# Kernel tuning notes

Hardware: AMD Instinct MI355X
Metric: run time of the kernel (lower is better)

The kernel has to match this reference:

```python
import jax, jax.numpy as jnp
import numpy as np

B, SQ, SK, H, HEADS, E, DFF = 4, 512, 1024, 1024, 16, 8, 4096
DH = H // HEADS
EPS = 1e-6


def _ln(x, g, b):
    m = jnp.mean(x, -1, keepdims=True)
    v = jnp.mean((x - m) ** 2, -1, keepdims=True)
    return (x - m) * jax.lax.rsqrt(v + EPS) * g + b


def setup_inputs() -> dict:
    key = jax.random.key(0)
    ks = jax.random.split(key, 16)
    s = 0.02
    return {
        "concated_input": jax.random.normal(ks[0], (B, SK, H), jnp.float32),
        "gen_emb": jax.random.normal(ks[1], (B, SQ, H), jnp.float32),
        "mask": jnp.zeros((B, 1, SQ, SK), jnp.float32),
        "ln_g": jnp.ones((H,), jnp.float32),
        "ln_b": jnp.zeros((H,), jnp.float32),
        "wq": jax.random.normal(ks[2], (H, H), jnp.float32) * s,
        "bq": jnp.zeros((H,), jnp.float32),
        "wk": jax.random.normal(ks[3], (H, H), jnp.float32) * s,
        "bk": jnp.zeros((H,), jnp.float32),
        "wv": jax.random.normal(ks[4], (H, H), jnp.float32) * s,
        "bv": jnp.zeros((H,), jnp.float32),
        "wo": jax.random.normal(ks[5], (H, H), jnp.float32) * s,
        "bo": jnp.zeros((H,), jnp.float32),
        "gw": jax.random.normal(ks[6], (H, E), jnp.float32) * s,
        "gb": jnp.zeros((E,), jnp.float32),
        "w1": jax.random.normal(ks[7], (E, H, DFF), jnp.float32) * s,
        "b1": jnp.zeros((E, DFF), jnp.float32),
        "w2": jax.random.normal(ks[8], (E, DFF, H), jnp.float32) * s,
        "b2": jnp.zeros((E, H), jnp.float32),
    }


def reference(concated_input, gen_emb, mask, ln_g, ln_b, wq, bq, wk, bk, wv, bv,
              wo, bo, gw, gb, w1, b1, w2, b2):
    residual_gen = gen_emb
    ctx_ln = _ln(concated_input, ln_g, ln_b)
    gen_ln = _ln(gen_emb, ln_g, ln_b)

    # multi-head cross attention: gen queries, concated keys/values
    q = (gen_ln @ wq + bq).reshape(B, SQ, HEADS, DH).transpose(0, 2, 1, 3)
    k = (ctx_ln @ wk + bk).reshape(B, SK, HEADS, DH).transpose(0, 2, 1, 3)
    v = (ctx_ln @ wv + bv).reshape(B, SK, HEADS, DH).transpose(0, 2, 1, 3)
    scores = jnp.einsum("bhqd,bhkd->bhqk", q, k) / np.sqrt(DH).astype(np.float32)
    attn = jax.nn.softmax(scores + mask, axis=-1)
    ctx_v = jnp.einsum("bhqk,bhkd->bhqd", attn, v)
    ctx_v = ctx_v.transpose(0, 2, 1, 3).reshape(B, SQ, H)
    ca_out = ctx_v @ wo + bo + residual_gen

    ln_ca = _ln(ca_out, ln_g, ln_b)

    # top-1 router on ca_out (pre-LN, as in original)
    gate = jax.nn.softmax(ca_out @ gw + gb, axis=-1)
    top_idx = jnp.argmax(gate, axis=-1)  # [B,SQ]

    # dense all-expert FFN, then gather selected expert (faithful to original)
    h1 = jax.nn.gelu(jnp.einsum("bsh,ehf->bsef", ln_ca, w1) + b1, approximate=False)
    expert_out = jnp.einsum("bsef,efh->bseh", h1, w2) + b2  # [B,SQ,E,H]
    sel = jnp.take_along_axis(expert_out, top_idx[:, :, None, None], axis=2)
    moe_out = sel[:, :, 0, :] + ln_ca
    return moe_out
```

## Files before the change

kernel.cpp:

```cpp
#include <hip/hip_runtime.h>
#include <stdint.h>
#include <stddef.h>

typedef _Float16 f16;
typedef _Float16 half8 __attribute__((ext_vector_type(8)));
typedef float f32x4 __attribute__((ext_vector_type(4)));

constexpr int kB = 4, kSQ = 512, kSK = 1024, kH = 1024, kHeads = 16, kE = 8, kDFF = 4096;
constexpr int kTok = kB * kSQ;

__device__ __forceinline__ void g2l16(const f16* g, f16* l) {
  __builtin_amdgcn_global_load_lds((const __attribute__((address_space(1))) uint32_t*)g,
                                   (__attribute__((address_space(3))) uint32_t*)l, 16, 0, 0);
}

__global__ __launch_bounds__(256) void tr_f2h(const float* __restrict__ src,
                                              f16* __restrict__ dst, int R, int C) {
  __shared__ float t[32][33];
  long zo = (long)blockIdx.z * R * C;
  int r0 = blockIdx.y * 32, c0 = blockIdx.x * 32;
  int tr = threadIdx.x >> 3, tc = (threadIdx.x & 7) << 2;
  float4 v = *(const float4*)(src + zo + (long)(r0 + tr) * C + c0 + tc);
  t[tr][tc] = v.x; t[tr][tc + 1] = v.y; t[tr][tc + 2] = v.z; t[tr][tc + 3] = v.w;
  __syncthreads();
  union { f16 h[4]; uint2 u; } o;
  o.h[0] = (f16)t[tc + 0][tr]; o.h[1] = (f16)t[tc + 1][tr];
  o.h[2] = (f16)t[tc + 2][tr]; o.h[3] = (f16)t[tc + 3][tr];
  *(uint2*)(dst + zo + (long)(c0 + tr) * R + r0 + tc) = o.u;
}

__global__ __launch_bounds__(256) void ln_kernel(const float* __restrict__ x,
                                                 const float* __restrict__ g,
                                                 const float* __restrict__ b,
                                                 f16* __restrict__ oh, float* __restrict__ of,
                                                 int rows) {
  int row = blockIdx.x;
  if (row >= rows) return;
  int tid = threadIdx.x;
  const float* xr = x + (long)row * kH;
  float4 v = *(const float4*)(xr + tid * 4);
  float s = v.x + v.y + v.z + v.w;
  float s2 = v.x * v.x + v.y * v.y + v.z * v.z + v.w * v.w;
  __shared__ float red[8];
  for (int o = 32; o; o >>= 1) { s += __shfl_down(s, o); s2 += __shfl_down(s2, o); }
  int wv = tid >> 6, lane = tid & 63;
  if (lane == 0) { red[wv] = s; red[4 + wv] = s2; }
  __syncthreads();
  if (tid == 0) {
    red[0] = red[0] + red[1] + red[2] + red[3];
    red[4] = red[4] + red[5] + red[6] + red[7];
  }
  __syncthreads();
  float mean = red[0] * (1.0f / kH);
  float var = red[4] * (1.0f / kH) - mean * mean;
  float rs = rsqrtf(var + 1e-6f);
  float4 gv = *(const float4*)(g + tid * 4);
  float4 bv = *(const float4*)(b + tid * 4);
  float y0 = (v.x - mean) * rs * gv.x + bv.x;
  float y1 = (v.y - mean) * rs * gv.y + bv.y;
  float y2 = (v.z - mean) * rs * gv.z + bv.z;
  float y3 = (v.w - mean) * rs * gv.w + bv.w;
  long base = (long)row * kH + tid * 4;
  if (oh) {
    union { f16 h[4]; uint2 u; } o;
    o.h[0] = (f16)y0; o.h[1] = (f16)y1; o.h[2] = (f16)y2; o.h[3] = (f16)y3;
    *(uint2*)(oh + base) = o.u;
  }
  if (of) { float4 o4 = {y0, y1, y2, y3}; *(float4*)(of + base) = o4; }
}

__global__ void zero_kernel(int* __restrict__ p, int n) {
  int i = blockIdx.x * blockDim.x + threadIdx.x;
  if (i < n) p[i] = 0;
}

__global__ __launch_bounds__(64) void router_kernel(const float* __restrict__ ca,
                                                    const float* __restrict__ gw,
                                                    const float* __restrict__ gb,
                                                    int* __restrict__ cursors,
                                                    int* __restrict__ list,
                                                    int* __restrict__ eid) {
  int t = blockIdx.x;
  int lane = threadIdx.x;
  const float* x = ca + (long)t * kH;
  float acc[kE];
#pragma unroll
  for (int e = 0; e < kE; e++) acc[e] = 0.0f;
  for (int h = lane; h < kH; h += 64) {
    float xv = x[h];
    const float* gr = gw + (long)h * kE;
#pragma unroll
    for (int e = 0; e < kE; e++) acc[e] += xv * gr[e];
  }
#pragma unroll
  for (int e = 0; e < kE; e++)
    for (int o = 32; o; o >>= 1) acc[e] += __shfl_down(acc[e], o);
  if (lane == 0) {
    int best = 0;
    float bv = acc[0] + gb[0];
    for (int e = 1; e < kE; e++) {
      float v = acc[e] + gb[e];
      if (v > bv) { bv = v; best = e; }
    }
    int slot = atomicAdd(&cursors[best], 1);
    list[best * kTok + slot] = t;
    eid[t] = best;
  }
}

__global__ __launch_bounds__(256) void ffn2_reduce(const float* __restrict__ part,
                                                   const float* __restrict__ lnca,
                                                   const float* __restrict__ b2,
                                                   const int* __restrict__ eid,
                                                   float* __restrict__ out) {
  int t = blockIdx.x;
  int i = threadIdx.x * 4;
  int e = eid[t];
  long idx = (long)t * kH + i;
  float4 p0 = *(const float4*)(part + idx);
  float4 p1 = *(const float4*)(part + (long)kTok * kH + idx);
  float4 p2 = *(const float4*)(part + 2L * kTok * kH + idx);
  float4 p3 = *(const float4*)(part + 3L * kTok * kH + idx);
  float4 r  = *(const float4*)(lnca + idx);
  float4 bb = *(const float4*)(b2 + (long)e * kH + i);
  float4 o = {p0.x + p1.x + p2.x + p3.x + r.x + bb.x,
              p0.y + p1.y + p2.y + p3.y + r.y + bb.y,
              p0.z + p1.z + p2.z + p3.z + r.z + bb.z,
              p0.w + p1.w + p2.w + p3.w + r.w + bb.w};
  *(float4*)(out + idx) = o;
}

__global__ __launch_bounds__(256) void flash_kernel(const f16* __restrict__ q,
                                                    const f16* __restrict__ k,
                                                    const f16* __restrict__ v_t,
                                                    const float* __restrict__ mask,
                                                    f16* __restrict__ ctx) {
  __shared__ f16 Ks[64 * 64];
  __shared__ f16 Vs[64 * 64];
  __shared__ f16 Ps[4][16][72];
  int qt = blockIdx.x;
  int bh = blockIdx.y;
  int b = bh >> 4;
  int ho = (bh & 15) * 64;
  int tid = threadIdx.x, lane = tid & 63, wave = tid >> 6;
  int quad = lane >> 4, lo = lane & 15;

  long qg = ((long)b * kSQ + qt * 64 + wave * 16 + lo) * kH + ho;
  half8 aq0 = *(const half8*)(q + qg + quad * 8);
  half8 aq1 = *(const half8*)(q + qg + 32 + quad * 8);

  int srow = tid >> 3;
  int soct = (tid & 7) ^ (srow & 7);
  const f16* ksrc[2];
  const f16* vsrc[2];
#pragma unroll
  for (int s = 0; s < 2; s++) {
    int r = s * 32 + srow;
    ksrc[s] = k + ((long)b * kSK + r) * kH + ho + soct * 8;
    vsrc[s] = v_t + ((long)bh * 64 + r) * kSK + soct * 8;
  }
  const float* maskp = mask + ((long)b * kSQ + qt * 64 + wave * 16 + quad * 4) * kSK;

  float m_s[4] = {-1e30f, -1e30f, -1e30f, -1e30f};
  float l_s[4] = {0.f, 0.f, 0.f, 0.f};
  f32x4 O[4] = {};

  for (int kt = 0; kt < kSK / 64; kt++) {
    int sk0 = kt * 64;
#pragma unroll
    for (int s = 0; s < 2; s++) g2l16(ksrc[s] + (long)sk0 * kH, &Ks[(s * 256 + tid) * 8]);
#pragma unroll
    for (int s = 0; s < 2; s++) g2l16(vsrc[s] + sk0, &Vs[(s * 256 + tid) * 8]);
    __syncthreads();
    f32x4 sf[4] = {};
#pragma unroll
    for (int nt = 0; nt < 4; nt++) {
      int key = nt * 16 + lo;
      half8 bk0 = *(const half8*)&Ks[key * 64 + (((0 * 4 + quad)) ^ (key & 7)) * 8];
      half8 bk1 = *(const half8*)&Ks[key * 64 + (((1 * 4 + quad)) ^ (key & 7)) * 8];
      sf[nt] = __builtin_amdgcn_mfma_f32_16x16x32_f16(aq0, bk0, sf[nt], 0, 0, 0);
      sf[nt] = __builtin_amdgcn_mfma_f32_16x16x32_f16(aq1, bk1, sf[nt], 0, 0, 0);
    }
#pragma unroll
    for (int r = 0; r < 4; r++)
#pragma unroll
      for (int nt = 0; nt < 4; nt++)
        sf[nt][r] += maskp[(long)r * kSK + sk0 + nt * 16 + lo];
#pragma unroll
    for (int r = 0; r < 4; r++) {
      float mx = fmaxf(fmaxf(sf[0][r], sf[1][r]), fmaxf(sf[2][r], sf[3][r]));
      mx = fmaxf(mx, __shfl_xor(mx, 1));
      mx = fmaxf(mx, __shfl_xor(mx, 2));
      mx = fmaxf(mx, __shfl_xor(mx, 4));
      mx = fmaxf(mx, __shfl_xor(mx, 8));
      float m_new = fmaxf(m_s[r], mx);
      float alpha = __expf(m_s[r] - m_new);
      m_s[r] = m_new;
      float p0 = __expf(sf[0][r] - m_new), p1 = __expf(sf[1][r] - m_new);
      float p2 = __expf(sf[2][r] - m_new), p3 = __expf(sf[3][r] - m_new);
      float rs = p0 + p1 + p2 + p3;
      rs += __shfl_xor(rs, 1);
      rs += __shfl_xor(rs, 2);
      rs += __shfl_xor(rs, 4);
      rs += __shfl_xor(rs, 8);
      l_s[r] = l_s[r] * alpha + rs;
#pragma unroll
      for (int nt = 0; nt < 4; nt++) O[nt][r] *= alpha;
      Ps[wave][quad * 4 + r][0 * 16 + lo] = (f16)p0;
      Ps[wave][quad * 4 + r][1 * 16 + lo] = (f16)p1;
      Ps[wave][quad * 4 + r][2 * 16 + lo] = (f16)p2;
      Ps[wave][quad * 4 + r][3 * 16 + lo] = (f16)p3;
    }
    half8 ap0 = *(const half8*)&Ps[wave][lo][quad * 8];
    half8 ap1 = *(const half8*)&Ps[wave][lo][32 + quad * 8];
#pragma unroll
    for (int nt = 0; nt < 4; nt++) {
      int d = nt * 16 + lo;
      half8 bv0 = *(const half8*)&Vs[d * 64 + (((0 * 4 + quad)) ^ (d & 7)) * 8];
      half8 bv1 = *(const half8*)&Vs[d * 64 + (((1 * 4 + quad)) ^ (d & 7)) * 8];
      O[nt] = __builtin_amdgcn_mfma_f32_16x16x32_f16(ap0, bv0, O[nt], 0, 0, 0);
      O[nt] = __builtin_amdgcn_mfma_f32_16x16x32_f16(ap1, bv1, O[nt], 0, 0, 0);
    }
    __syncthreads();
  }
#pragma unroll
  for (int r = 0; r < 4; r++) {
    float inv = 1.0f / l_s[r];
    long row = (long)b * kSQ + qt * 64 + wave * 16 + quad * 4 + r;
#pragma unroll
    for (int nt = 0; nt < 4; nt++)
      ctx[row * kH + ho + nt * 16 + lo] = (f16)(O[nt][r] * inv);
  }
}

struct GemmP {
  const f16* A; long a_row, a_z1, a_z2;
  const f16* Bm; long b_nstr, b_z1, b_z2;
  float* Cf; f16* Ch; long c_row, c_z1, c_z2, c_split; int c_tr;
  const float* bias; long bias_z;
  const float* res; long res_row, res_z1, res_z2;
  float alpha; int gelu; int ksplit;
  int M, N, K, zdiv;
  const int* glist; const int* cnt;
};

template <int BM, int BN>
__device__ __forceinline__ void gemm_body(const GemmP& p, int bx, int by, int bz,
                                          f16* A0, f16* A1, f16* B0, f16* B1) {
  constexpr int FM = BM / 32, FN = BN / 32;
  int z = bz;
  int kb = 0, kEnd = p.K, ks = 0;
  if (p.ksplit > 1) {
    int kc = p.K / p.ksplit;
    ks = z % p.ksplit;
    kb = ks * kc;
    kEnd = kb + kc;
    z /= p.ksplit;
  }
  long aoff = 0, boff = 0, coff = 0, roff = 0, biasoff = 0;
  const int* gl = nullptr;
  int Meff = p.M;
  if (p.glist) {
    Meff = p.cnt[z];
    gl = p.glist + (long)z * kTok;
    boff = (long)z * p.b_z2;
    biasoff = (long)z * p.bias_z;
  } else {
    int z1 = z / p.zdiv, z2 = z % p.zdiv;
    aoff = (long)z1 * p.a_z1 + (long)z2 * p.a_z2;
    boff = (long)z1 * p.b_z1 + (long)z2 * p.b_z2;
    coff = (long)z1 * p.c_z1 + (long)z2 * p.c_z2;
    roff = (long)z1 * p.res_z1 + (long)z2 * p.res_z2;
  }
  coff += (long)ks * p.c_split;
  int m0 = by * BM;
  if (m0 >= Meff) return;
  int n0 = bx * BN;
  int tid = threadIdx.x, lane = tid & 63, wave = tid >> 6;
  int wm = (wave & 1) * (BM / 2), wn = (wave >> 1) * (BN / 2);
  int q = lane >> 4, lo = lane & 15;

  int srow = tid >> 3;
  int soct = (tid & 7) ^ (srow & 7);
  const f16* asrc[BM / 32];
  const f16* bsrc[BN / 32];
#pragma unroll
  for (int s = 0; s < BM / 32; s++) {
    int row = m0 + s * 32 + srow;
    if (gl) row = gl[row < Meff ? row : Meff - 1];
    asrc[s] = p.A + aoff + (long)row * p.a_row + soct * 8;
  }
#pragma unroll
  for (int s = 0; s < BN / 32; s++)
    bsrc[s] = p.Bm + boff + (long)(n0 + s * 32 + srow) * p.b_nstr + soct * 8;

  f32x4 acc[FM][FN] = {};

  auto stage = [&](f16* Ad, f16* Bd, int k0) {
#pragma unroll
    for (int s = 0; s < BM / 32; s++) g2l16(asrc[s] + k0, &Ad[(s * 256 + tid) * 8]);
#pragma unroll
    for (int s = 0; s < BN / 32; s++) g2l16(bsrc[s] + k0, &Bd[(s * 256 + tid) * 8]);
  };
  auto compute = [&](const f16* As, const f16* Bs) {
    half8 af[2][FM], bf[2][FN];
#pragma unroll
    for (int kk = 0; kk < 2; kk++) {
#pragma unroll
      for (int i = 0; i < FM; i++) {
        int r = wm + i * 16 + lo;
        af[kk][i] = *(const half8*)&As[r * 64 + ((kk * 4 + q) ^ (r & 7)) * 8];
      }
#pragma unroll
      for (int j = 0; j < FN; j++) {
        int n = wn + j * 16 + lo;
        bf[kk][j] = *(const half8*)&Bs[n * 64 + ((kk * 4 + q) ^ (n & 7)) * 8];
      }
    }
#pragma unroll
    for (int kk = 0; kk < 2; kk++)
#pragma unroll
      for (int i = 0; i < FM; i++)
#pragma unroll
        for (int j = 0; j < FN; j++)
          acc[i][j] = __builtin_amdgcn_mfma_f32_16x16x32_f16(af[kk][i], bf[kk][j], acc[i][j], 0, 0, 0);
  };

  stage(A0, B0, kb);
  __syncthreads();
  for (int k0 = kb; k0 < kEnd; k0 += 128) {
    if (k0 + 64 < kEnd) stage(A1, B1, k0 + 64);
    compute(A0, B0);
    __syncthreads();
    if (k0 + 64 < kEnd) {
      if (k0 + 128 < kEnd) stage(A0, B0, k0 + 128);
      compute(A1, B1);
      __syncthreads();
    }
  }

#pragma unroll
  for (int i = 0; i < FM; i++) {
#pragma unroll
    for (int j = 0; j < FN; j++) {
      int col = n0 + wn + j * 16 + lo;
      if (p.c_tr) {
        int row0 = m0 + wm + i * 16 + q * 4;
        union { f16 h[4]; uint2 u; } o;
#pragma unroll
        for (int r = 0; r < 4; r++) {
          float v = acc[i][j][r];
          if (p.bias) v += p.bias[biasoff + col];
          v *= p.alpha;
          o.h[r] = (f16)v;
        }
        *(uint2*)&p.Ch[coff + (long)col * p.c_row + row0] = o.u;
      } else {
#pragma unroll
        for (int r = 0; r < 4; r++) {
          int row = m0 + wm + i * 16 + q * 4 + r;
          if (row < Meff) {
            long rr = gl ? (long)gl[row] : (long)row;
            float v = acc[i][j][r];
            if (p.bias) v += p.bias[biasoff + col];
            v *= p.alpha;
            if (p.res) v += p.res[roff + rr * p.res_row + col];
            if (p.gelu) v = 0.5f * v * (1.0f + erff(v * 0.70710678118654752f));
            long ci = coff + rr * p.c_row + col;
            if (p.Cf) p.Cf[ci] = v;
            else p.Ch[ci] = (f16)v;
          }
        }
      }
    }
  }
}

template <int BM, int BN>
__global__ __launch_bounds__(256) void gemm_t(GemmP p) {
  __shared__ f16 A0[BM * 64], A1[BM * 64], B0[BN * 64], B1[BN * 64];
  gemm_body<BM, BN>(p, blockIdx.x, blockIdx.y, blockIdx.z, A0, A1, B0, B1);
}

struct Multi3P {
  GemmP g0, g1, g2;
  int n0, n1;
  int gx0, gy0, gx1, gy1, gx2, gy2;
};

__global__ __launch_bounds__(256) void gemm_qkv(Multi3P mp) {
  __shared__ f16 A0[128 * 64], A1[128 * 64], B0[128 * 64], B1[128 * 64];
  int fb = blockIdx.x;
  if (fb < mp.n0) {
    gemm_body<128, 128>(mp.g0, fb % mp.gx0, (fb / mp.gx0) % mp.gy0, fb / (mp.gx0 * mp.gy0),
                        A0, A1, B0, B1);
    return;
  }
  fb -= mp.n0;
  if (fb < mp.n1) {
    gemm_body<128, 128>(mp.g1, fb % mp.gx1, (fb / mp.gx1) % mp.gy1, fb / (mp.gx1 * mp.gy1),
                        A0, A1, B0, B1);
    return;
  }
  fb -= mp.n1;
  gemm_body<128, 128>(mp.g2, fb % mp.gx2, (fb / mp.gx2) % mp.gy2, fb / (mp.gx2 * mp.gy2),
                      A0, A1, B0, B1);
}

extern "C" void kernel_launch(void* const* d_in, const int* in_sizes, int n_in,
                              void* d_out, int out_size, void* d_ws, size_t ws_size,
                              hipStream_t stream) {
  const float* concated = (const float*)d_in[0];
  const float* gen      = (const float*)d_in[1];
  const float* mask     = (const float*)d_in[2];
  const float* ln_g     = (const float*)d_in[3];
  const float* ln_b     = (const float*)d_in[4];
  const float* wq = (const float*)d_in[5];  const float* bq = (const float*)d_in[6];
  const float* wk = (const float*)d_in[7];  const float* bk = (const float*)d_in[8];
  const float* wv = (const float*)d_in[9];  const float* bv = (const float*)d_in[10];
  const float* wo = (const float*)d_in[11]; const float* bo = (const float*)d_in[12];
  const float* gw = (const float*)d_in[13]; const float* gb = (const float*)d_in[14];
  const float* w1 = (const float*)d_in[15]; const float* b1 = (const float*)d_in[16];
  const float* w2 = (const float*)d_in[17]; const float* b2 = (const float*)d_in[18];
  float* out = (float*)d_out;

  size_t off = 0;
  auto alloc = [&](size_t bytes) -> void* {
    void* p = (char*)d_ws + off;
    off += (bytes + 255) & ~(size_t)255;
    return p;
  };
  f16* wq_t  = (f16*)alloc((size_t)kH * kH * 2);
  f16* wk_t  = (f16*)alloc((size_t)kH * kH * 2);
  f16* wv_t  = (f16*)alloc((size_t)kH * kH * 2);
  f16* wo_t  = (f16*)alloc((size_t)kH * kH * 2);
  f16* w1_t  = (f16*)alloc((size_t)kE * kH * kDFF * 2);
  f16* w2_t  = (f16*)alloc((size_t)kE * kDFF * kH * 2);
  f16* lnc_h = (f16*)alloc((size_t)kB * kSK * kH * 2);
  f16* lng_h = (f16*)alloc((size_t)kTok * kH * 2);
  f16* q_h   = (f16*)alloc((size_t)kTok * kH * 2);
  f16* k_h   = (f16*)alloc((size_t)kB * kSK * kH * 2);
  f16* v_t   = (f16*)alloc((size_t)kB * kSK * kH * 2);
  f16* ctx_h = (f16*)alloc((size_t)kTok * kH * 2);
  float* ca_f   = (float*)alloc((size_t)kTok * kH * 4);
  float* lnca_f = (float*)alloc((size_t)kTok * kH * 4);
  f16* lnca_h   = (f16*)alloc((size_t)kTok * kH * 2);
  f16* h1_h     = (f16*)alloc((size_t)kTok * kDFF * 2);
  float* part_f = (float*)alloc((size_t)4 * kTok * kH * 4);
  int* cnt_d    = (int*)alloc(kE * 4);
  int* list_d   = (int*)alloc((size_t)kE * kTok * 4);
  int* eid_d    = (int*)alloc((size_t)kTok * 4);

  tr_f2h<<<dim3(32, 32, 1), 256, 0, stream>>>(wq, wq_t, kH, kH);
  tr_f2h<<<dim3(32, 32, 1), 256, 0, stream>>>(wk, wk_t, kH, kH);
  tr_f2h<<<dim3(32, 32, 1), 256, 0, stream>>>(wv, wv_t, kH, kH);
  tr_f2h<<<dim3(32, 32, 1), 256, 0, stream>>>(wo, wo_t, kH, kH);
  tr_f2h<<<dim3(kDFF / 32, kH / 32, kE), 256, 0, stream>>>(w1, w1_t, kH, kDFF);
  tr_f2h<<<dim3(kH / 32, kDFF / 32, kE), 256, 0, stream>>>(w2, w2_t, kDFF, kH);

  ln_kernel<<<kB * kSK, 256, 0, stream>>>(concated, ln_g, ln_b, lnc_h, nullptr, kB * kSK);
  ln_kernel<<<kTok, 256, 0, stream>>>(gen, ln_g, ln_b, lng_h, nullptr, kTok);

  {
    Multi3P mp{};
    GemmP& pq = mp.g0;
    pq.A = lng_h; pq.a_row = kH; pq.Bm = wq_t; pq.b_nstr = kH;
    pq.Ch = q_h; pq.c_row = kH; pq.bias = bq; pq.alpha = 0.125f;
    pq.M = kTok; pq.N = kH; pq.K = kH; pq.zdiv = 1;
    GemmP& pk = mp.g1;
    pk.A = lnc_h; pk.a_row = kH; pk.Bm = wk_t; pk.b_nstr = kH;
    pk.Ch = k_h; pk.c_row = kH; pk.bias = bk; pk.alpha = 1.0f;
    pk.M = kB * kSK; pk.N = kH; pk.K = kH; pk.zdiv = 1;
    GemmP& pv = mp.g2;
    pv.A = lnc_h; pv.a_row = kH; pv.a_z1 = (long)kSK * kH;
    pv.Bm = wv_t; pv.b_nstr = kH;
    pv.Ch = v_t; pv.c_row = kSK; pv.c_z1 = (long)kH * kSK; pv.c_tr = 1;
    pv.bias = bv; pv.alpha = 1.0f;
    pv.M = kSK; pv.N = kH; pv.K = kH; pv.zdiv = 1;
    mp.gx0 = kH / 128; mp.gy0 = kTok / 128;        mp.n0 = mp.gx0 * mp.gy0;
    mp.gx1 = kH / 128; mp.gy1 = (kB * kSK) / 128;  mp.n1 = mp.gx1 * mp.gy1;
    mp.gx2 = kH / 128; mp.gy2 = kSK / 128;
    int ntot = mp.n0 + mp.n1 + mp.gx2 * mp.gy2 * kB;
    gemm_qkv<<<dim3(ntot), 256, 0, stream>>>(mp);
  }
  flash_kernel<<<dim3(kSQ / 64, kB * kHeads), 256, 0, stream>>>(q_h, k_h, v_t, mask, ctx_h);
  {
    GemmP p{}; p.A = ctx_h; p.a_row = kH;
    p.Bm = wo_t; p.b_nstr = kH;
    p.Cf = ca_f; p.c_row = kH; p.bias = bo;
    p.res = gen; p.res_row = kH;
    p.alpha = 1.0f; p.M = kTok; p.N = kH; p.K = kH; p.zdiv = 1;
    gemm_t<64, 64><<<dim3(kH / 64, kTok / 64, 1), 256, 0, stream>>>(p);
  }
  ln_kernel<<<kTok, 256, 0, stream>>>(ca_f, ln_g, ln_b, lnca_h, lnca_f, kTok);
  zero_kernel<<<1, 64, 0, stream>>>(cnt_d, kE);
  router_kernel<<<kTok, 64, 0, stream>>>(ca_f, gw, gb, cnt_d, list_d, eid_d);
  {
    GemmP p{}; p.A = lnca_h; p.a_row = kH;
    p.Bm = w1_t; p.b_nstr = kH; p.b_z2 = (long)kH * kDFF;
    p.Ch = h1_h; p.c_row = kDFF; p.bias = b1; p.bias_z = kDFF;
    p.alpha = 1.0f; p.gelu = 1; p.M = kTok; p.N = kDFF; p.K = kH; p.zdiv = 1;
    p.glist = list_d; p.cnt = cnt_d;
    gemm_t<128, 128><<<dim3(kDFF / 128, kTok / 128, kE), 256, 0, stream>>>(p);
  }
  {
    GemmP p{}; p.A = h1_h; p.a_row = kDFF;
    p.Bm = w2_t; p.b_nstr = kDFF; p.b_z2 = (long)kDFF * kH;
    p.Cf = part_f; p.c_row = kH; p.c_split = (long)kTok * kH;
    p.alpha = 1.0f; p.ksplit = 4;
    p.M = kTok; p.N = kH; p.K = kDFF; p.zdiv = 1;
    p.glist = list_d; p.cnt = cnt_d;
    gemm_t<128, 128><<<dim3(kH / 128, kTok / 128, kE * 4), 256, 0, stream>>>(p);
  }
  ffn2_reduce<<<kTok, 256, 0, stream>>>(part_f, lnca_f, b2, eid_d, out);
}
```

Baseline: 690.1 us.

## Triple-buffer GEMM K-loop with vmcnt waits and switch tiles to 128x64

Replaces the double-buffered K loop, which had two full barriers per pair of stages, with a three-buffer ring. Each iteration issues loads two tiles ahead, waits on the vmcnt counter only for the current tile, and uses a single barrier. All GEMM launches move to 128x64 tiles, which gives more blocks and keeps LDS use near the old 128x128 double-buffered footprint. The aim is deeper load/compute overlap and better occupancy. The cost is half the MMA work per B-tile load and a hand-counted vmcnt that must match the number of loads issued per stage.

```diff
diff --git a/kernel.cpp b/kernel.cpp
--- a/kernel.cpp
+++ b/kernel.cpp
@@ -12,6 +12,11 @@
 __device__ __forceinline__ void g2l16(const f16* g, f16* l) {
   __builtin_amdgcn_global_load_lds((const __attribute__((address_space(1))) uint32_t*)g,
                                    (__attribute__((address_space(3))) uint32_t*)l, 16, 0, 0);
+}
+
+template <int N>
+__device__ __forceinline__ void vmwait() {
+  asm volatile("s_waitcnt vmcnt(%0)" :: "i"(N) : "memory");
 }
 
 __global__ __launch_bounds__(256) void tr_f2h(const float* __restrict__ src,
@@ -246,8 +251,10 @@
 
 template <int BM, int BN>
 __device__ __forceinline__ void gemm_body(const GemmP& p, int bx, int by, int bz,
-                                          f16* A0, f16* A1, f16* B0, f16* B1) {
+                                          f16* A0, f16* A1, f16* A2,
+                                          f16* B0, f16* B1, f16* B2) {
   constexpr int FM = BM / 32, FN = BN / 32;
+  constexpr int PER = BM / 32 + BN / 32;
   int z = bz;
   int kb = 0, kEnd = p.K, ks = 0;
   if (p.ksplit > 1) {
@@ -326,17 +333,20 @@
           acc[i][j] = __builtin_amdgcn_mfma_f32_16x16x32_f16(af[kk][i], bf[kk][j], acc[i][j], 0, 0, 0);
   };
 
+  int nt = (kEnd - kb) / 64;
   stage(A0, B0, kb);
-  __syncthreads();
-  for (int k0 = kb; k0 < kEnd; k0 += 128) {
-    if (k0 + 64 < kEnd) stage(A1, B1, k0 + 64);
-    compute(A0, B0);
-    __syncthreads();
-    if (k0 + 64 < kEnd) {
-      if (k0 + 128 < kEnd) stage(A0, B0, k0 + 128);
-      compute(A1, B1);
-      __syncthreads();
-    }
+  if (nt > 1) stage(A1, B1, kb + 64);
+  f16 *Ac = A0, *An = A1, *Af = A2;
+  f16 *Bc = B0, *Bn = B1, *Bf = B2;
+  for (int i = 0; i < nt; i++) {
+    if (i + 1 < nt) vmwait<PER>(); else vmwait<0>();
+    __builtin_amdgcn_sched_barrier(0);
+    __builtin_amdgcn_s_barrier();
+    if (i + 2 < nt) stage(Af, Bf, kb + (i + 2) * 64);
+    compute(Ac, Bc);
+    f16* t;
+    t = Ac; Ac = An; An = Af; Af = t;
+    t = Bc; Bc = Bn; Bn = Bf; Bf = t;
   }
 
 #pragma unroll
@@ -378,8 +388,9 @@
 
 template <int BM, int BN>
 __global__ __launch_bounds__(256) void gemm_t(GemmP p) {
-  __shared__ f16 A0[BM * 64], A1[BM * 64], B0[BN * 64], B1[BN * 64];
-  gemm_body<BM, BN>(p, blockIdx.x, blockIdx.y, blockIdx.z, A0, A1, B0, B1);
+  __shared__ f16 A0[BM * 64], A1[BM * 64], A2[BM * 64];
+  __shared__ f16 B0[BN * 64], B1[BN * 64], B2[BN * 64];
+  gemm_body<BM, BN>(p, blockIdx.x, blockIdx.y, blockIdx.z, A0, A1, A2, B0, B1, B2);
 }
 
 struct Multi3P {
@@ -389,22 +400,23 @@
 };
 
 __global__ __launch_bounds__(256) void gemm_qkv(Multi3P mp) {
-  __shared__ f16 A0[128 * 64], A1[128 * 64], B0[128 * 64], B1[128 * 64];
+  __shared__ f16 A0[128 * 64], A1[128 * 64], A2[128 * 64];
+  __shared__ f16 B0[64 * 64], B1[64 * 64], B2[64 * 64];
   int fb = blockIdx.x;
   if (fb < mp.n0) {
-    gemm_body<128, 128>(mp.g0, fb % mp.gx0, (fb / mp.gx0) % mp.gy0, fb / (mp.gx0 * mp.gy0),
-                        A0, A1, B0, B1);
+    gemm_body<128, 64>(mp.g0, fb % mp.gx0, (fb / mp.gx0) % mp.gy0, fb / (mp.gx0 * mp.gy0),
+                       A0, A1, A2, B0, B1, B2);
     return;
   }
   fb -= mp.n0;
   if (fb < mp.n1) {
-    gemm_body<128, 128>(mp.g1, fb % mp.gx1, (fb / mp.gx1) % mp.gy1, fb / (mp.gx1 * mp.gy1),
-                        A0, A1, B0, B1);
+    gemm_body<128, 64>(mp.g1, fb % mp.gx1, (fb / mp.gx1) % mp.gy1, fb / (mp.gx1 * mp.gy1),
+                       A0, A1, A2, B0, B1, B2);
     return;
   }
   fb -= mp.n1;
-  gemm_body<128, 128>(mp.g2, fb % mp.gx2, (fb / mp.gx2) % mp.gy2, fb / (mp.gx2 * mp.gy2),
-                      A0, A1, B0, B1);
+  gemm_body<128, 64>(mp.g2, fb % mp.gx2, (fb / mp.gx2) % mp.gy2, fb / (mp.gx2 * mp.gy2),
+                     A0, A1, A2, B0, B1, B2);
 }
 
 extern "C" void kernel_launch(void* const* d_in, const int* in_sizes, int n_in,
@@ -477,9 +489,9 @@
     pv.Ch = v_t; pv.c_row = kSK; pv.c_z1 = (long)kH * kSK; pv.c_tr = 1;
     pv.bias = bv; pv.alpha = 1.0f;
     pv.M = kSK; pv.N = kH; pv.K = kH; pv.zdiv = 1;
-    mp.gx0 = kH / 128; mp.gy0 = kTok / 128;        mp.n0 = mp.gx0 * mp.gy0;
-    mp.gx1 = kH / 128; mp.gy1 = (kB * kSK) / 128;  mp.n1 = mp.gx1 * mp.gy1;
-    mp.gx2 = kH / 128; mp.gy2 = kSK / 128;
+    mp.gx0 = kH / 64; mp.gy0 = kTok / 128;        mp.n0 = mp.gx0 * mp.gy0;
+    mp.gx1 = kH / 64; mp.gy1 = (kB * kSK) / 128;  mp.n1 = mp.gx1 * mp.gy1;
+    mp.gx2 = kH / 64; mp.gy2 = kSK / 128;
     int ntot = mp.n0 + mp.n1 + mp.gx2 * mp.gy2 * kB;
     gemm_qkv<<<dim3(ntot), 256, 0, stream>>>(mp);
   }
@@ -490,7 +502,7 @@
     p.Cf = ca_f; p.c_row = kH; p.bias = bo;
     p.res = gen; p.res_row = kH;
     p.alpha = 1.0f; p.M = kTok; p.N = kH; p.K = kH; p.zdiv = 1;
-    gemm_t<64, 64><<<dim3(kH / 64, kTok / 64, 1), 256, 0, stream>>>(p);
+    gemm_t<128, 64><<<dim3(kH / 64, kTok / 128, 1), 256, 0, stream>>>(p);
   }
   ln_kernel<<<kTok, 256, 0, stream>>>(ca_f, ln_g, ln_b, lnca_h, lnca_f, kTok);
   zero_kernel<<<1, 64, 0, stream>>>(cnt_d, kE);
@@ -501,7 +513,7 @@
     p.Ch = h1_h; p.c_row = kDFF; p.bias = b1; p.bias_z = kDFF;
     p.alpha = 1.0f; p.gelu = 1; p.M = kTok; p.N = kDFF; p.K = kH; p.zdiv = 1;
     p.glist = list_d; p.cnt = cnt_d;
-    gemm_t<128, 128><<<dim3(kDFF / 128, kTok / 128, kE), 256, 0, stream>>>(p);
+    gemm_t<128, 64><<<dim3(kDFF / 64, kTok / 128, kE), 256, 0, stream>>>(p);
   }
   {
     GemmP p{}; p.A = h1_h; p.a_row = kDFF;
@@ -510,7 +522,7 @@
     p.alpha = 1.0f; p.ksplit = 4;
     p.M = kTok; p.N = kH; p.K = kDFF; p.zdiv = 1;
     p.glist = list_d; p.cnt = cnt_d;
-    gemm_t<128, 128><<<dim3(kH / 128, kTok / 128, kE * 4), 256, 0, stream>>>(p);
+    gemm_t<128, 64><<<dim3(kH / 64, kTok / 128, kE * 4), 256, 0, stream>>>(p);
   }
   ffn2_reduce<<<kTok, 256, 0, stream>>>(part_f, lnca_f, b2, eid_d, out);
 }
```

Measured after the change: 728.9 us. 1.06x slower.
